# Optimization experiments

Measured on AMD Instinct MI355X. Metric: run time of the kernel, lower is better.

The kernel has to match this reference:

```python
import jax, jax.numpy as jnp
import numpy as np

V, D, H, L, FF, NC = 32000, 512, 8, 4, 2048, 10
HD = D // H
EPS = 1e-5


def _layernorm(x, g, b):
    m = jnp.mean(x, axis=-1, keepdims=True)
    v = jnp.mean((x - m) ** 2, axis=-1, keepdims=True)
    return (x - m) * jax.lax.rsqrt(v + EPS) * g + b


def _pos_encoding(T, d):
    pos = jnp.arange(T, dtype=jnp.float32)[:, None]
    div = jnp.exp(jnp.arange(0, d, 2, dtype=jnp.float32) * (-np.log(10000.0) / d))
    pe = jnp.zeros((T, d), dtype=jnp.float32)
    pe = pe.at[:, 0::2].set(jnp.sin(pos * div))
    pe = pe.at[:, 1::2].set(jnp.cos(pos * div))
    return pe


def setup_inputs() -> dict:
    key = jax.random.key(0)
    ks = iter(jax.random.split(key, 32))
    n = lambda shape, s=0.02: jax.random.normal(next(ks), shape, dtype=jnp.float32) * s
    inp = {
        "tokens": jax.random.randint(next(ks), (8, 1024), 0, V),
        "emb": n((V, D), 1.0),
        # attention projections, stored (in, out) so y = x @ W + b
        "Wq": n((L, D, D)), "bq": jnp.zeros((L, D)),
        "Wk": n((L, D, D)), "bk": jnp.zeros((L, D)),
        "Wv": n((L, D, D)), "bv": jnp.zeros((L, D)),
        "Wo": n((L, D, D)), "bo": jnp.zeros((L, D)),
        "ln1_g": jnp.ones((L, D)), "ln1_b": jnp.zeros((L, D)),
        "ln2_g": jnp.ones((L, D)), "ln2_b": jnp.zeros((L, D)),
        "W1": n((L, D, FF)), "b1": jnp.zeros((L, FF)),
        "W2": n((L, FF, D)), "b2": jnp.zeros((L, D)),
        "heavy_w": n((D, D)), "heavy_b": jnp.zeros((D,)),
        "heavy_a1": n((D, D)), "heavy_a2": n((D, D)),
        "norm_g": jnp.ones((D,)), "norm_b": jnp.zeros((D,)),
        "cls_W": n((D, NC)), "cls_b": jnp.zeros((NC,)),
    }
    return inp


def reference(tokens, emb, Wq, bq, Wk, bk, Wv, bv, Wo, bo,
              ln1_g, ln1_b, ln2_g, ln2_b, W1, b1, W2, b2,
              heavy_w, heavy_b, heavy_a1, heavy_a2,
              norm_g, norm_b, cls_W, cls_b):
    B, T = tokens.shape
    x = emb[tokens] + _pos_encoding(T, D)[None]  # [B,T,D]
    scale = 1.0 / np.sqrt(HD)
    for l in range(L):
        # attention block (pre-norm)
        h = _layernorm(x, ln1_g[l], ln1_b[l])
        q = (h @ Wq[l] + bq[l]).reshape(B, T, H, HD)
        k = (h @ Wk[l] + bk[l]).reshape(B, T, H, HD)
        v = (h @ Wv[l] + bv[l]).reshape(B, T, H, HD)
        scores = jnp.einsum("bqhd,bkhd->bhqk", q, k) * scale
        attn = jax.nn.softmax(scores, axis=-1)
        o = jnp.einsum("bhqk,bkhd->bqhd", attn, v).reshape(B, T, D)
        x = x + (o @ Wo[l] + bo[l])
        # feedforward block
        h = _layernorm(x, ln2_g[l], ln2_b[l])
        x = x + (jax.nn.gelu(h @ W1[l] + b1[l], approximate=False) @ W2[l] + b2[l])
    # heavy layer: chained matmuls + bias + tanh (vectorized over B*T)
    x = jnp.tanh(((x @ heavy_w) @ heavy_a1) @ heavy_a2 + heavy_b)
    x = _layernorm(x, norm_g, norm_b)
    x = jnp.mean(x, axis=1)  # [B,D]
    return x @ cls_W + cls_b  # [B,NC]
```

## Files before the change

### kernel.cpp

```cpp
#include <hip/hip_runtime.h>
#include <math.h>

#define BS   8
#define TT   1024
#define DD   512
#define HH   8
#define LL   4
#define FFD  2048
#define NCC  10
#define MM   (BS*TT)
#define MDl  ((long)MM*DD)

typedef unsigned short u16;
typedef short  short8 __attribute__((ext_vector_type(8)));
typedef float  f32x4  __attribute__((ext_vector_type(4)));
typedef u16    u16x8  __attribute__((ext_vector_type(8)));
typedef u16    u16x4  __attribute__((ext_vector_type(4)));

static __device__ __forceinline__ u16 f2b(float f) {
    union { float f; unsigned u; } x; x.f = f;
    unsigned r = x.u + 0x7FFFu + ((x.u >> 16) & 1u);
    return (u16)(r >> 16);
}
static __device__ __forceinline__ u16 f2b_fast(float f) {
    union { float f; unsigned u; } x; x.f = f;
    return (u16)((x.u + 0x8000u) >> 16);
}
static __device__ __forceinline__ float b2f(u16 u) {
    union { unsigned u; float f; } x; x.u = ((unsigned)u) << 16;
    return x.f;
}

__global__ __launch_bounds__(256)
void embed_kernel(const int* __restrict__ tok, const float* __restrict__ emb,
                  float* __restrict__ X) {
    int i = blockIdx.x * 256 + threadIdx.x;
    int d = i & (DD - 1);
    int row = i >> 9;
    int t = row & (TT - 1);
    int j = d >> 1;
    float freq = __expf((float)(2 * j) * (-9.210340371976184f / 512.0f));
    float ang = (float)t * freq;
    float pe = (d & 1) ? cosf(ang) : sinf(ang);
    X[i] = emb[(long)tok[row] * DD + d] + pe;
}

template<int OUTBF>
__global__ __launch_bounds__(256)
void ln_kernel(const float* __restrict__ in, void* __restrict__ outp,
               const float* __restrict__ g, const float* __restrict__ b) {
    int row = blockIdx.x;
    int tid = threadIdx.x;
    const float* x = in + (long)row * DD;
    float x1 = x[tid], x2 = x[tid + 256];
    __shared__ float red[256], red2[256];
    red[tid] = x1 + x2;
    red2[tid] = x1 * x1 + x2 * x2;
    __syncthreads();
    for (int st = 128; st > 0; st >>= 1) {
        if (tid < st) { red[tid] += red[tid + st]; red2[tid] += red2[tid + st]; }
        __syncthreads();
    }
    float mean = red[0] * (1.0f / DD);
    float var = red2[0] * (1.0f / DD) - mean * mean;
    float rstd = rsqrtf(var + 1e-5f);
    float y1 = (x1 - mean) * rstd * g[tid] + b[tid];
    float y2 = (x2 - mean) * rstd * g[tid + 256] + b[tid + 256];
    if (OUTBF) {
        u16* o = (u16*)outp + (long)row * DD;
        o[tid] = f2b(y1); o[tid + 256] = f2b(y2);
    } else {
        float* o = (float*)outp + (long)row * DD;
        o[tid] = y1; o[tid + 256] = y2;
    }
}

template<int OUTBF, int HAS_BIAS, int ACT, int HAS_RES>
__global__ __launch_bounds__(512, 2)
void mfma_gemm(const u16* __restrict__ A, const u16* __restrict__ BT,
               const float* __restrict__ bias, const float* __restrict__ R,
               void* __restrict__ Cout, int N, int K) {
    __shared__ __align__(16) u16 lds[17408];
    u16* As = lds;
    u16* Bs = lds + 8192;
    const int tid = threadIdx.x;
    const int lane = tid & 63;
    const int w = tid >> 6;
    const int wm = w >> 1;
    const int wn = w & 1;
    const long bm = (long)blockIdx.y * 128;
    const long bn = (long)blockIdx.x * 128;

    f32x4 acc[2][4];
#pragma unroll
    for (int i = 0; i < 2; ++i)
#pragma unroll
        for (int j = 0; j < 4; ++j) acc[i][j] = {0.f, 0.f, 0.f, 0.f};

    const int srow = tid >> 2;
    const int sc0 = (tid & 3) * 2;
    const u16* Ag = A + (bm + srow) * K + sc0 * 8;
    const u16* Bg = BT + (bn + srow) * K + sc0 * 8;
    int soff[2];
#pragma unroll
    for (int j = 0; j < 2; ++j)
        soff[j] = srow * 64 + ((sc0 + j) ^ (srow & 7)) * 8;

    const int fr = lane & 15;
    const int g = lane >> 4;
    const int am0 = wm * 32 + fr;
    const int bn0 = wn * 64 + fr;
    const int sw = fr & 7;

    u16x8 sa[2][2], sb[2][2];
#pragma unroll
    for (int j = 0; j < 2; ++j) {
        sa[0][j] = *(const u16x8*)(Ag + j * 8);
        sb[0][j] = *(const u16x8*)(Bg + j * 8);
    }

    for (int k0 = 0; k0 < K; k0 += 128) {
#pragma unroll
        for (int half = 0; half < 2; ++half) {
            const int cb = half, nb = half ^ 1;
            __syncthreads();
#pragma unroll
            for (int j = 0; j < 2; ++j) {
                *(u16x8*)&As[soff[j]] = sa[cb][j];
                *(u16x8*)&Bs[soff[j]] = sb[cb][j];
            }
            const int knext = k0 + (half + 1) * 64;
            if (knext < K) {
#pragma unroll
                for (int j = 0; j < 2; ++j) {
                    sa[nb][j] = *(const u16x8*)(Ag + knext + j * 8);
                    sb[nb][j] = *(const u16x8*)(Bg + knext + j * 8);
                }
            }
            __syncthreads();
#pragma unroll
            for (int kk = 0; kk < 2; ++kk) {
                const int pos = ((kk << 2) + g) ^ sw;
                short8 af[2], bfv[4];
#pragma unroll
                for (int mi = 0; mi < 2; ++mi)
                    af[mi] = *(const short8*)&As[(am0 + mi * 16) * 64 + pos * 8];
#pragma unroll
                for (int ni = 0; ni < 4; ++ni)
                    bfv[ni] = *(const short8*)&Bs[(bn0 + ni * 16) * 64 + pos * 8];
#pragma unroll
                for (int mi = 0; mi < 2; ++mi)
#pragma unroll
                    for (int ni = 0; ni < 4; ++ni)
                        acc[mi][ni] = __builtin_amdgcn_mfma_f32_16x16x32_bf16(
                            af[mi], bfv[ni], acc[mi][ni], 0, 0, 0);
            }
        }
    }

    const int erow0 = wm * 32 + g * 4;
    const int ecol0 = wn * 64 + fr;

    if (OUTBF) {
        __syncthreads();
#pragma unroll
        for (int ni = 0; ni < 4; ++ni) {
            const long col = bn + ecol0 + ni * 16;
            float bv = 0.f;
            if (HAS_BIAS) bv = bias[col];
#pragma unroll
            for (int mi = 0; mi < 2; ++mi)
#pragma unroll
                for (int r = 0; r < 4; ++r) {
                    const int row = erow0 + mi * 16 + r;
                    float v = acc[mi][ni][r];
                    if (HAS_BIAS) v += bv;
                    if (ACT == 1) v = 0.5f * v * (1.0f + erff(v * 0.70710678118654752f));
                    if (ACT == 2) v = tanhf(v);
                    if (HAS_RES) v += R[(bm + row) * N + col];
                    lds[row * 136 + ecol0 + ni * 16] = f2b(v);
                }
        }
        __syncthreads();
        const int srow2 = tid >> 4;
        const int sch2 = tid & 15;
        u16* Cp = (u16*)Cout;
#pragma unroll
        for (int rr = 0; rr < 4; ++rr) {
            const int row = srow2 + rr * 32;
            u16x8 vv = *(const u16x8*)&lds[row * 136 + sch2 * 8];
            *(u16x8*)(Cp + (bm + row) * N + bn + sch2 * 8) = vv;
        }
    } else {
#pragma unroll
        for (int ni = 0; ni < 4; ++ni) {
            const long col = bn + ecol0 + ni * 16;
            float bv = 0.f;
            if (HAS_BIAS) bv = bias[col];
#pragma unroll
            for (int mi = 0; mi < 2; ++mi)
#pragma unroll
                for (int r = 0; r < 4; ++r) {
                    const long row = bm + erow0 + mi * 16 + r;
                    float v = acc[mi][ni][r];
                    if (HAS_BIAS) v += bv;
                    if (ACT == 1) v = 0.5f * v * (1.0f + erff(v * 0.70710678118654752f));
                    if (ACT == 2) v = tanhf(v);
                    if (HAS_RES) v += R[row * N + col];
                    ((float*)Cout)[row * N + col] = v;
                }
        }
    }
}

__global__ __launch_bounds__(256, 4)
void attn_kernel(const u16* __restrict__ QKV, u16* __restrict__ O) {
    const int id = blockIdx.x;
    const int bh = ((id >> 7) << 3) | (id & 7);
    const int qblk = (id >> 3) & 15;
    const int h = bh & 7;
    const int b = bh >> 3;
    const int tid = threadIdx.x;
    const int lane = tid & 63;
    const int w = tid >> 6;
    const int fr = lane & 15;
    const int g = lane >> 4;
    const int q8 = g * 8;

    __shared__ __align__(16) u16 Ks[64 * 64];
    __shared__ __align__(16) u16 Vt[64 * 72];
    __shared__ __align__(16) u16 Pw[4][16 * 72];

    const long rowb = (long)b * TT;
    const int wq0 = qblk * 64 + w * 16;

    short8 qf[2];
#pragma unroll
    for (int hf = 0; hf < 2; ++hf)
        qf[hf] = *(const short8*)(QKV + (rowb + wq0 + fr) * 1536
                                  + h * 64 + hf * 32 + q8);

    f32x4 accO[4];
    float lsum[4];
#pragma unroll
    for (int nt = 0; nt < 4; ++nt) accO[nt] = {0.f, 0.f, 0.f, 0.f};
#pragma unroll
    for (int r = 0; r < 4; ++r) lsum[r] = 0.f;

    const int skey = tid >> 2;
    const int skc = (tid & 3) * 2;
    const int koff0 = skey * 64 + ((skc ^ (skey & 7)) * 8);
    const int koff1 = skey * 64 + (((skc + 1) ^ (skey & 7)) * 8);
    const int vkp = tid & 31;
    const int vd0 = (tid >> 5) * 8;

    auto load_kv = [&](int kt_, u16x8* kr_, u16x8* vr_) {
        const long tb_ = (rowb + (long)kt_ * 64) * 1536 + h * 64;
        const u16* kp_ = QKV + tb_ + 512 + (long)skey * 1536 + skc * 8;
        kr_[0] = *(const u16x8*)kp_;
        kr_[1] = *(const u16x8*)(kp_ + 8);
        const u16* vp_ = QKV + tb_ + 1024 + (long)(vkp * 2) * 1536 + vd0;
        vr_[0] = *(const u16x8*)vp_;
        vr_[1] = *(const u16x8*)(vp_ + 1536);
    };
    auto stage = [&](u16x8* kr_, u16x8* vr_) {
        *(u16x8*)&Ks[koff0] = kr_[0];
        *(u16x8*)&Ks[koff1] = kr_[1];
        unsigned* Vt32 = (unsigned*)Vt;
#pragma unroll
        for (int j = 0; j < 8; ++j)
            Vt32[(vd0 + j) * 36 + vkp] =
                (unsigned)vr_[0][j] | ((unsigned)vr_[1][j] << 16);
    };
    auto compute = [&]() {
        f32x4 accS[4];
#pragma unroll
        for (int n = 0; n < 4; ++n) accS[n] = {0.f, 0.f, 0.f, 0.f};
#pragma unroll
        for (int n = 0; n < 4; ++n)
#pragma unroll
            for (int hf = 0; hf < 2; ++hf) {
                short8 bk = *(const short8*)&Ks[(n * 16 + fr) * 64
                                                + ((((hf << 2) + g) ^ (fr & 7)) * 8)];
                accS[n] = __builtin_amdgcn_mfma_f32_16x16x32_bf16(qf[hf], bk, accS[n], 0, 0, 0);
            }
#pragma unroll
        for (int r = 0; r < 4; ++r) {
            int prow = g * 4 + r;
#pragma unroll
            for (int n = 0; n < 4; ++n) {
                float pv = exp2f(accS[n][r] * 0.18033688011112042f);
                lsum[r] += pv;
                Pw[w][prow * 72 + n * 16 + fr] = f2b_fast(pv);
            }
        }
#pragma unroll
        for (int hf = 0; hf < 2; ++hf) {
            short8 pa = *(const short8*)&Pw[w][fr * 72 + hf * 32 + q8];
#pragma unroll
            for (int nt = 0; nt < 4; ++nt) {
                short8 bv = *(const short8*)&Vt[(nt * 16 + fr) * 72 + hf * 32 + q8];
                accO[nt] = __builtin_amdgcn_mfma_f32_16x16x32_bf16(pa, bv, accO[nt], 0, 0, 0);
            }
        }
    };

    u16x8 krA[2], vrA[2], krB[2], vrB[2];
    load_kv(0, krA, vrA);

#pragma unroll 1
    for (int kt = 0; kt < 16; kt += 2) {
        __syncthreads();
        stage(krA, vrA);
        load_kv(kt + 1, krB, vrB);
        __syncthreads();
        compute();
        __syncthreads();
        stage(krB, vrB);
        if (kt + 2 < 16) load_kv(kt + 2, krA, vrA);
        __syncthreads();
        compute();
    }

#pragma unroll
    for (int r = 0; r < 4; ++r) {
        float s = lsum[r];
        s += __shfl_xor(s, 1, 64);
        s += __shfl_xor(s, 2, 64);
        s += __shfl_xor(s, 4, 64);
        s += __shfl_xor(s, 8, 64);
        lsum[r] = 1.0f / s;
    }
#pragma unroll
    for (int nt = 0; nt < 4; ++nt)
#pragma unroll
        for (int r = 0; r < 4; ++r) {
            long row = rowb + wq0 + g * 4 + r;
            O[row * DD + h * 64 + nt * 16 + fr] = f2b(accO[nt][r] * lsum[r]);
        }
}

struct WP   { const float* s; u16* d; };
struct WTbl { WP e[19]; };

__global__ __launch_bounds__(256)
void wprep512_kernel(WTbl tbl) {
    const float* src = tbl.e[blockIdx.z].s;
    u16* dst = tbl.e[blockIdx.z].d;
    int k0 = blockIdx.y * 32, n0 = blockIdx.x * 32;
    __shared__ float tile[32][33];
    int tx = threadIdx.x & 31, ty = threadIdx.x >> 5;
#pragma unroll
    for (int i = 0; i < 4; ++i)
        tile[ty + 8 * i][tx] = src[(long)(k0 + ty + 8 * i) * 512 + n0 + tx];
    __syncthreads();
#pragma unroll
    for (int i = 0; i < 4; ++i) {
        int r = ty + 8 * i;
        dst[(long)(n0 + r) * 512 + k0 + tx] = f2b(tile[tx][r]);
    }
}

__global__ __launch_bounds__(256)
void wprep_kernel(const float* __restrict__ src, u16* __restrict__ dst,
                  int K, int N, long srcLS, long dstLS) {
    int l = blockIdx.z;
    src += (long)l * srcLS;
    dst += (long)l * dstLS;
    int k0 = blockIdx.y * 32, n0 = blockIdx.x * 32;
    __shared__ float tile[32][33];
    int tx = threadIdx.x & 31, ty = threadIdx.x >> 5;
#pragma unroll
    for (int i = 0; i < 4; ++i)
        tile[ty + 8 * i][tx] = src[(long)(k0 + ty + 8 * i) * N + n0 + tx];
    __syncthreads();
#pragma unroll
    for (int i = 0; i < 4; ++i) {
        int r = ty + 8 * i;
        dst[(long)(n0 + r) * K + k0 + tx] = f2b(tile[tx][r]);
    }
}

__global__ __launch_bounds__(256)
void bprep_kernel(const float* __restrict__ bq, const float* __restrict__ bk,
                  const float* __restrict__ bv, float* __restrict__ dst) {
    int i = blockIdx.x * 256 + threadIdx.x;
    int l = i / 1536, j = i - l * 1536;
    float v = (j < 512) ? bq[l * 512 + j]
            : (j < 1024) ? bk[l * 512 + j - 512]
                         : bv[l * 512 + j - 1024];
    dst[i] = v;
}

__global__ __launch_bounds__(256)
void f2b_kernel(const float* __restrict__ in, u16* __restrict__ out, int n) {
    int i = blockIdx.x * 256 + threadIdx.x;
    if (i < n) out[i] = f2b(in[i]);
}

__global__ __launch_bounds__(256)
void zero_kernel(float* __restrict__ p, int n) {
    int i = blockIdx.x * 256 + threadIdx.x;
    if (i < n) p[i] = 0.0f;
}

__global__ __launch_bounds__(256)
void colmean_kernel(const float* __restrict__ Hn, float* __restrict__ XM) {
    int blk = blockIdx.x;
    int b = blk >> 5;
    int r0 = (blk & 31) * 32;
    int tid = threadIdx.x;
    float acc0 = 0.0f, acc1 = 0.0f;
    for (int r = 0; r < 32; ++r) {
        long off = ((long)b * TT + r0 + r) * DD + tid;
        acc0 += Hn[off];
        acc1 += Hn[off + 256];
    }
    atomicAdd(&XM[b * DD + tid], acc0);
    atomicAdd(&XM[b * DD + tid + 256], acc1);
}

__global__ __launch_bounds__(256)
void cls_kernel(const float* __restrict__ XM, const float* __restrict__ W,
                const float* __restrict__ bias, float* __restrict__ out) {
    int b = blockIdx.x;
    int tid = threadIdx.x;
    __shared__ float xm[DD];
    xm[tid] = XM[b * DD + tid] * (1.0f / TT);
    xm[tid + 256] = XM[b * DD + tid + 256] * (1.0f / TT);
    __syncthreads();
    if (tid < NCC) {
        float s = bias[tid];
        for (int d = 0; d < DD; ++d) s += xm[d] * W[d * NCC + tid];
        out[b * NCC + tid] = s;
    }
}

extern "C" void kernel_launch(void* const* d_in, const int* in_sizes, int n_in,
                              void* d_out, int out_size, void* d_ws, size_t ws_size,
                              hipStream_t stream) {
    const int*   tokens  = (const int*)d_in[0];
    const float* emb     = (const float*)d_in[1];
    const float* Wq      = (const float*)d_in[2];
    const float* bq      = (const float*)d_in[3];
    const float* Wk      = (const float*)d_in[4];
    const float* bk      = (const float*)d_in[5];
    const float* Wv      = (const float*)d_in[6];
    const float* bv      = (const float*)d_in[7];
    const float* Wo      = (const float*)d_in[8];
    const float* bo      = (const float*)d_in[9];
    const float* ln1_g   = (const float*)d_in[10];
    const float* ln1_b   = (const float*)d_in[11];
    const float* ln2_g   = (const float*)d_in[12];
    const float* ln2_b   = (const float*)d_in[13];
    const float* W1      = (const float*)d_in[14];
    const float* b1      = (const float*)d_in[15];
    const float* W2      = (const float*)d_in[16];
    const float* b2      = (const float*)d_in[17];
    const float* heavy_w = (const float*)d_in[18];
    const float* heavy_b = (const float*)d_in[19];
    const float* heavy_a1= (const float*)d_in[20];
    const float* heavy_a2= (const float*)d_in[21];
    const float* norm_g  = (const float*)d_in[22];
    const float* norm_b  = (const float*)d_in[23];
    const float* cls_W   = (const float*)d_in[24];
    const float* cls_b   = (const float*)d_in[25];
    float* out = (float*)d_out;

    char* p = (char*)d_ws;
    float* X    = (float*)p;  p += MDl * 4;
    u16*   Hh   = (u16*)p;    p += MDl * 2;
    u16*   QKVb = (u16*)p;
    u16*   FFb  = QKVb;
    u16*   T1   = QKVb;
    u16*   T2   = QKVb + MDl;
    float* LNout= (float*)QKVb;
    p += (long)MM * 1536 * 2;
    u16*   Ob   = (u16*)p;    p += MDl * 2;
    u16*   Xbf  = (u16*)p;    p += MDl * 2;
    u16*   WqkvT= (u16*)p;    p += 4L * 1536 * 512 * 2;
    u16*   WoT  = (u16*)p;    p += 4L * 512 * 512 * 2;
    u16*   W1T  = (u16*)p;    p += 4L * 2048 * 512 * 2;
    u16*   W2T  = (u16*)p;    p += 4L * 512 * 2048 * 2;
    u16*   WhT  = (u16*)p;    p += 3L * 512 * 512 * 2;
    float* bqkv = (float*)p;  p += 4L * 1536 * 4;
    float* XM   = (float*)p;  p += (long)BS * DD * 4;

    dim3 blk(256);
    dim3 blk512(512);

    WTbl tbl;
    for (int l = 0; l < 4; ++l) {
        tbl.e[l * 4 + 0] = {Wq + (long)l * 262144, WqkvT + (long)l * 786432};
        tbl.e[l * 4 + 1] = {Wk + (long)l * 262144, WqkvT + (long)l * 786432 + 262144};
        tbl.e[l * 4 + 2] = {Wv + (long)l * 262144, WqkvT + (long)l * 786432 + 524288};
        tbl.e[l * 4 + 3] = {Wo + (long)l * 262144, WoT + (long)l * 262144};
    }
    tbl.e[16] = {heavy_w,  WhT};
    tbl.e[17] = {heavy_a1, WhT + 262144};
    tbl.e[18] = {heavy_a2, WhT + 524288};
    wprep512_kernel<<<dim3(16, 16, 19), blk, 0, stream>>>(tbl);
    wprep_kernel<<<dim3(64, 16, 4), blk, 0, stream>>>(W1, W1T,  512, 2048, 1048576, 1048576);
    wprep_kernel<<<dim3(16, 64, 4), blk, 0, stream>>>(W2, W2T, 2048,  512, 1048576, 1048576);
    bprep_kernel<<<24, blk, 0, stream>>>(bq, bk, bv, bqkv);

    embed_kernel<<<MM * DD / 256, blk, 0, stream>>>(tokens, emb, X);

    dim3 gQKV(12, 64), g512(4, 64), gFF1(16, 64);

    for (int l = 0; l < LL; ++l) {
        ln_kernel<1><<<MM, blk, 0, stream>>>(X, Hh, ln1_g + l * DD, ln1_b + l * DD);
        mfma_gemm<1, 1, 0, 0><<<gQKV, blk512, 0, stream>>>(
            Hh, WqkvT + (long)l * 786432, bqkv + l * 1536, nullptr, QKVb, 1536, 512);
        attn_kernel<<<dim3(1024), blk, 0, stream>>>(QKVb, Ob);
        mfma_gemm<0, 1, 0, 1><<<g512, blk512, 0, stream>>>(
            Ob, WoT + (long)l * 262144, bo + l * DD, X, X, 512, 512);
        ln_kernel<1><<<MM, blk, 0, stream>>>(X, Hh, ln2_g + l * DD, ln2_b + l * DD);
        mfma_gemm<1, 1, 1, 0><<<gFF1, blk512, 0, stream>>>(
            Hh, W1T + (long)l * 1048576, b1 + l * FFD, nullptr, FFb, 2048, 512);
        mfma_gemm<0, 1, 0, 1><<<g512, blk512, 0, stream>>>(
            FFb, W2T + (long)l * 1048576, b2 + l * DD, X, X, 512, 2048);
    }

    f2b_kernel<<<MM * DD / 256, blk, 0, stream>>>(X, Xbf, MM * DD);
    mfma_gemm<1, 0, 0, 0><<<g512, blk512, 0, stream>>>(Xbf, WhT,          nullptr, nullptr, T1, 512, 512);
    mfma_gemm<1, 0, 0, 0><<<g512, blk512, 0, stream>>>(T1,  WhT + 262144, nullptr, nullptr, T2, 512, 512);
    mfma_gemm<0, 1, 2, 0><<<g512, blk512, 0, stream>>>(T2,  WhT + 524288, heavy_b, nullptr, X,  512, 512);

    ln_kernel<0><<<MM, blk, 0, stream>>>(X, LNout, norm_g, norm_b);
    zero_kernel<<<(BS * DD + 255) / 256, blk, 0, stream>>>(XM, BS * DD);
    colmean_kernel<<<256, blk, 0, stream>>>(LNout, XM);
    cls_kernel<<<BS, blk, 0, stream>>>(XM, cls_W, cls_b, out);
}
```

Measured before the change: 888.7 us.

## Split attention keys across waves with register-resident probabilities and final cross-wave reduction

Attention is restructured so each wave holds all 64 queries of the block and processes its own 16-key slice of every key tile. Scores are computed transposed (K·Qᵀ), so the exponentiated probabilities already sit in the MFMA operand layout. That removes the per-wave P round trip through shared memory and all block-wide barriers inside the key loop; V is staged into per-wave private double buffers. In exchange, the PV MFMAs run with half of the K dimension zero-padded, register use grows (launch bounds drop from 4 to 2 blocks), and an extra cross-wave reduction of outputs and row sums through shared memory is added at the end.

```diff
diff --git a/kernel.cpp b/kernel.cpp
--- a/kernel.cpp
+++ b/kernel.cpp
@@ -213,7 +213,7 @@
     }
 }
 
-__global__ __launch_bounds__(256, 4)
+__global__ __launch_bounds__(256, 2)
 void attn_kernel(const u16* __restrict__ QKV, u16* __restrict__ O) {
     const int id = blockIdx.x;
     const int bh = ((id >> 7) << 3) | (id & 7);
@@ -225,119 +225,138 @@
     const int w = tid >> 6;
     const int fr = lane & 15;
     const int g = lane >> 4;
-    const int q8 = g * 8;
-
-    __shared__ __align__(16) u16 Ks[64 * 64];
-    __shared__ __align__(16) u16 Vt[64 * 72];
-    __shared__ __align__(16) u16 Pw[4][16 * 72];
+
+    __shared__ __align__(16) unsigned char smem[20480];
+    u16* Vt = (u16*)smem;
+    float (*Ored)[16][68] = (float(*)[16][68])smem;
+    __shared__ float Lred[4][4][16];
 
     const long rowb = (long)b * TT;
-    const int wq0 = qblk * 64 + w * 16;
-
-    short8 qf[2];
-#pragma unroll
-    for (int hf = 0; hf < 2; ++hf)
-        qf[hf] = *(const short8*)(QKV + (rowb + wq0 + fr) * 1536
-                                  + h * 64 + hf * 32 + q8);
-
-    f32x4 accO[4];
+    const int q0 = qblk * 64;
+
+    short8 qf[4][2];
+#pragma unroll
+    for (int qt = 0; qt < 4; ++qt)
+#pragma unroll
+        for (int hf = 0; hf < 2; ++hf)
+            qf[qt][hf] = *(const short8*)(QKV + (rowb + q0 + qt * 16 + fr) * 1536
+                                          + h * 64 + hf * 32 + g * 8);
+
+    f32x4 accO[4][4];
     float lsum[4];
 #pragma unroll
-    for (int nt = 0; nt < 4; ++nt) accO[nt] = {0.f, 0.f, 0.f, 0.f};
-#pragma unroll
-    for (int r = 0; r < 4; ++r) lsum[r] = 0.f;
-
-    const int skey = tid >> 2;
-    const int skc = (tid & 3) * 2;
-    const int koff0 = skey * 64 + ((skc ^ (skey & 7)) * 8);
-    const int koff1 = skey * 64 + (((skc + 1) ^ (skey & 7)) * 8);
-    const int vkp = tid & 31;
-    const int vd0 = (tid >> 5) * 8;
-
-    auto load_kv = [&](int kt_, u16x8* kr_, u16x8* vr_) {
-        const long tb_ = (rowb + (long)kt_ * 64) * 1536 + h * 64;
-        const u16* kp_ = QKV + tb_ + 512 + (long)skey * 1536 + skc * 8;
-        kr_[0] = *(const u16x8*)kp_;
-        kr_[1] = *(const u16x8*)(kp_ + 8);
-        const u16* vp_ = QKV + tb_ + 1024 + (long)(vkp * 2) * 1536 + vd0;
-        vr_[0] = *(const u16x8*)vp_;
-        vr_[1] = *(const u16x8*)(vp_ + 1536);
+    for (int qt = 0; qt < 4; ++qt) {
+        lsum[qt] = 0.f;
+#pragma unroll
+        for (int nt = 0; nt < 4; ++nt) accO[qt][nt] = {0.f, 0.f, 0.f, 0.f};
+    }
+
+    const int vkp = lane & 7;
+    const int vd0 = (lane >> 3) * 8;
+    u16* Vw0 = Vt + w * 2560;
+
+    auto load_k = [&](int kt_, u16x8* kr_) {
+        const u16* kp = QKV + (rowb + (long)kt_ * 64 + w * 16 + fr) * 1536
+                        + 512 + h * 64 + g * 8;
+        kr_[0] = *(const u16x8*)kp;
+        kr_[1] = *(const u16x8*)(kp + 32);
     };
-    auto stage = [&](u16x8* kr_, u16x8* vr_) {
-        *(u16x8*)&Ks[koff0] = kr_[0];
-        *(u16x8*)&Ks[koff1] = kr_[1];
-        unsigned* Vt32 = (unsigned*)Vt;
+    auto load_v = [&](int kt_, u16x8* vr_) {
+        const u16* vp = QKV + (rowb + (long)kt_ * 64 + w * 16 + vkp * 2) * 1536
+                        + 1024 + h * 64 + vd0;
+        vr_[0] = *(const u16x8*)vp;
+        vr_[1] = *(const u16x8*)(vp + 1536);
+    };
+    auto stage_v = [&](int buf, u16x8* vr_) {
+        unsigned* Vt32 = (unsigned*)(Vw0 + buf * 1280);
 #pragma unroll
         for (int j = 0; j < 8; ++j)
-            Vt32[(vd0 + j) * 36 + vkp] =
+            Vt32[(vd0 + j) * 10 + vkp] =
                 (unsigned)vr_[0][j] | ((unsigned)vr_[1][j] << 16);
     };
-    auto compute = [&]() {
-        f32x4 accS[4];
-#pragma unroll
-        for (int n = 0; n < 4; ++n) accS[n] = {0.f, 0.f, 0.f, 0.f};
-#pragma unroll
-        for (int n = 0; n < 4; ++n)
-#pragma unroll
-            for (int hf = 0; hf < 2; ++hf) {
-                short8 bk = *(const short8*)&Ks[(n * 16 + fr) * 64
-                                                + ((((hf << 2) + g) ^ (fr & 7)) * 8)];
-                accS[n] = __builtin_amdgcn_mfma_f32_16x16x32_bf16(qf[hf], bk, accS[n], 0, 0, 0);
-            }
-#pragma unroll
-        for (int r = 0; r < 4; ++r) {
-            int prow = g * 4 + r;
-#pragma unroll
-            for (int n = 0; n < 4; ++n) {
-                float pv = exp2f(accS[n][r] * 0.18033688011112042f);
-                lsum[r] += pv;
-                Pw[w][prow * 72 + n * 16 + fr] = f2b_fast(pv);
-            }
-        }
-#pragma unroll
-        for (int hf = 0; hf < 2; ++hf) {
-            short8 pa = *(const short8*)&Pw[w][fr * 72 + hf * 32 + q8];
-#pragma unroll
-            for (int nt = 0; nt < 4; ++nt) {
-                short8 bv = *(const short8*)&Vt[(nt * 16 + fr) * 72 + hf * 32 + q8];
-                accO[nt] = __builtin_amdgcn_mfma_f32_16x16x32_bf16(pa, bv, accO[nt], 0, 0, 0);
-            }
+    auto compute = [&](int buf, u16x8* kr_) {
+        const u16* Vw = Vw0 + buf * 1280;
+        short8 vb[4];
+#pragma unroll
+        for (int nt = 0; nt < 4; ++nt) {
+            union { short8 s; u16x4 h2[2]; } u;
+            u.h2[0] = *(const u16x4*)(Vw + (nt * 16 + fr) * 20 + g * 4);
+            u.h2[1] = (u16x4){0, 0, 0, 0};
+            vb[nt] = u.s;
+        }
+#pragma unroll
+        for (int qt = 0; qt < 4; ++qt) {
+            f32x4 st = {0.f, 0.f, 0.f, 0.f};
+            st = __builtin_amdgcn_mfma_f32_16x16x32_bf16(kr_[0], qf[qt][0], st, 0, 0, 0);
+            st = __builtin_amdgcn_mfma_f32_16x16x32_bf16(kr_[1], qf[qt][1], st, 0, 0, 0);
+            u16 p0 = f2b_fast(exp2f(st[0] * 0.18033688011112042f));
+            u16 p1 = f2b_fast(exp2f(st[1] * 0.18033688011112042f));
+            u16 p2 = f2b_fast(exp2f(st[2] * 0.18033688011112042f));
+            u16 p3 = f2b_fast(exp2f(st[3] * 0.18033688011112042f));
+            lsum[qt] += (b2f(p0) + b2f(p1)) + (b2f(p2) + b2f(p3));
+            union { short8 s; unsigned u[4]; } pu;
+            pu.u[0] = (unsigned)p0 | ((unsigned)p1 << 16);
+            pu.u[1] = (unsigned)p2 | ((unsigned)p3 << 16);
+            pu.u[2] = 0; pu.u[3] = 0;
+#pragma unroll
+            for (int nt = 0; nt < 4; ++nt)
+                accO[qt][nt] = __builtin_amdgcn_mfma_f32_16x16x32_bf16(
+                    pu.s, vb[nt], accO[qt][nt], 0, 0, 0);
         }
     };
 
     u16x8 krA[2], vrA[2], krB[2], vrB[2];
-    load_kv(0, krA, vrA);
+    load_k(0, krA); load_v(0, vrA);
+    load_k(1, krB); load_v(1, vrB);
+    stage_v(0, vrA);
 
 #pragma unroll 1
     for (int kt = 0; kt < 16; kt += 2) {
+        stage_v(1, vrB);
+        compute(0, krA);
+        if (kt + 2 < 16) { load_k(kt + 2, krA); load_v(kt + 2, vrA); }
+        compute(1, krB);
+        if (kt + 2 < 16) {
+            stage_v(0, vrA);
+            load_k(kt + 3, krB); load_v(kt + 3, vrB);
+        }
+    }
+
+#pragma unroll
+    for (int qt = 0; qt < 4; ++qt) {
+        float s = lsum[qt];
+        s += __shfl_xor(s, 16, 64);
+        s += __shfl_xor(s, 32, 64);
+        Lred[w][qt][fr] = s;
+    }
+    __syncthreads();
+
+    const int q_ = tid >> 4;
+    const int d0 = (tid & 15) * 4;
+#pragma unroll 1
+    for (int qt = 0; qt < 4; ++qt) {
+#pragma unroll
+        for (int nt = 0; nt < 4; ++nt)
+#pragma unroll
+            for (int r = 0; r < 4; ++r)
+                Ored[w][g * 4 + r][nt * 16 + fr] = accO[qt][nt][r];
         __syncthreads();
-        stage(krA, vrA);
-        load_kv(kt + 1, krB, vrB);
+        f32x4 s = {0.f, 0.f, 0.f, 0.f};
+#pragma unroll
+        for (int ww = 0; ww < 4; ++ww) {
+            f32x4 t = *(const f32x4*)&Ored[ww][q_][d0];
+            s[0] += t[0]; s[1] += t[1]; s[2] += t[2]; s[3] += t[3];
+        }
+        float ltot = Lred[0][qt][q_] + Lred[1][qt][q_]
+                   + Lred[2][qt][q_] + Lred[3][qt][q_];
+        float rls = 1.0f / ltot;
+        long row = rowb + q0 + qt * 16 + q_;
+        u16x4 ov;
+#pragma unroll
+        for (int j = 0; j < 4; ++j) ov[j] = f2b(s[j] * rls);
+        *(u16x4*)(O + row * DD + h * 64 + d0) = ov;
         __syncthreads();
-        compute();
-        __syncthreads();
-        stage(krB, vrB);
-        if (kt + 2 < 16) load_kv(kt + 2, krA, vrA);
-        __syncthreads();
-        compute();
-    }
-
-#pragma unroll
-    for (int r = 0; r < 4; ++r) {
-        float s = lsum[r];
-        s += __shfl_xor(s, 1, 64);
-        s += __shfl_xor(s, 2, 64);
-        s += __shfl_xor(s, 4, 64);
-        s += __shfl_xor(s, 8, 64);
-        lsum[r] = 1.0f / s;
-    }
-#pragma unroll
-    for (int nt = 0; nt < 4; ++nt)
-#pragma unroll
-        for (int r = 0; r < 4; ++r) {
-            long row = rowb + wq0 + g * 4 + r;
-            O[row * DD + h * 64 + nt * 16 + fr] = f2b(accO[nt][r] * lsum[r]);
-        }
+    }
 }
 
 struct WP   { const float* s; u16* d; };
```

Measured after the change: 961.5 us. +8.2%, slower.
